# Performance work log

Hardware: AMD Instinct MI355X
Metric: run time of the kernel (lower is better)

Reference implementation:

```python
import jax, jax.numpy as jnp
import numpy as np

N = 8192
IN_F = 256
OUT_F = 256
ATTN_DIM = 2
NEG_INF = -1e18


def setup_inputs() -> dict:
    key = jax.random.key(0)
    k1, k2, k3, k4, k5 = jax.random.split(key, 5)
    node_feats = jax.random.normal(k1, (N, IN_F), dtype=jnp.float32)
    Ahat = (jax.random.uniform(k2, (N, N)) < 0.01).astype(jnp.float32)
    # ensure no isolated rows (self loops) so softmax rows are well-defined
    Ahat = Ahat.at[jnp.arange(N), jnp.arange(N)].set(1.0)
    bound_w = 1.0 / np.sqrt(IN_F)
    bound_wa = 1.0 / np.sqrt(OUT_F)
    bound_a = 1.0 / np.sqrt(2 * ATTN_DIM)
    w = jax.random.uniform(k3, (IN_F, OUT_F), minval=-bound_w, maxval=bound_w, dtype=jnp.float32)
    w_a = jax.random.uniform(k4, (OUT_F, ATTN_DIM), minval=-bound_wa, maxval=bound_wa, dtype=jnp.float32)
    a = jax.random.uniform(k5, (2 * ATTN_DIM, 1), minval=-bound_a, maxval=bound_a, dtype=jnp.float32)
    return {"node_feats": node_feats, "Ahat": Ahat, "w": w, "w_a": w_a, "a": a}


def reference(node_feats, Ahat, w, w_a, a):
    # h_prime: [N, out_features]
    h_prime = node_feats @ w
    # h_reduced: [N, attn_dim]
    h_reduced = h_prime @ w_a
    # e[i, j] = cat(h_red[i], h_red[j]) @ a  ==  h_red[i]@a[:d] + h_red[j]@a[d:]
    # (identical math to the repeat+cat+matmul in the original, without the
    #  O(N^2 * 2d) materialization)
    f_src = (h_reduced @ a[:ATTN_DIM]).squeeze(-1)  # [N]
    f_dst = (h_reduced @ a[ATTN_DIM:]).squeeze(-1)  # [N]
    e = f_src[:, None] + f_dst[None, :]             # [N, N]
    masked_e = jnp.where(Ahat > 0, e, NEG_INF)
    attn_scores = jax.nn.softmax(masked_e, axis=-1)  # [N, N]
    out = attn_scores @ h_prime                      # [N, out_features]
    return jax.nn.relu(out)
```

## Files before the change

### kernel.cpp

```cpp
#include <hip/hip_runtime.h>
#include <hip/hip_bf16.h>
#include <math.h>

#define NN 8192
#define IN_F 256
#define OUT_F 256

typedef _Float16 half4_t __attribute__((ext_vector_type(4)));
typedef float    f4_t    __attribute__((ext_vector_type(4)));

#define KC 32
#define LS 68

__global__ __launch_bounds__(256) void gemm_hprime(
    const float* __restrict__ X,
    const float* __restrict__ W,
    _Float16* __restrict__ H16)
{
    __shared__ float As[KC * LS];
    __shared__ float Bs[KC * LS];

    const int tid  = threadIdx.x;
    const int row0 = blockIdx.x * 64;
    const int col0 = blockIdx.y * 64;
    const int tx   = tid & 15;
    const int ty   = tid >> 4;

    float acc[4][4];
#pragma unroll
    for (int i = 0; i < 4; ++i)
#pragma unroll
        for (int j = 0; j < 4; ++j) acc[i][j] = 0.0f;

    for (int k0 = 0; k0 < IN_F; k0 += KC) {
        {
            const int k4 = tid & 7;
            const int r0 = tid >> 3;
#pragma unroll
            for (int rp = 0; rp < 2; ++rp) {
                const int r = r0 + rp * 32;
                const float4 v = *(const float4*)(X + (size_t)(row0 + r) * IN_F + k0 + k4 * 4);
                As[(k4 * 4 + 0) * LS + r] = v.x;
                As[(k4 * 4 + 1) * LS + r] = v.y;
                As[(k4 * 4 + 2) * LS + r] = v.z;
                As[(k4 * 4 + 3) * LS + r] = v.w;
            }
        }
        {
            const int c4 = tid & 15;
            const int kb = tid >> 4;
#pragma unroll
            for (int kp = 0; kp < 2; ++kp) {
                const int k = kb + kp * 16;
                *(float4*)(&Bs[k * LS + c4 * 4]) =
                    *(const float4*)(W + (size_t)(k0 + k) * OUT_F + col0 + c4 * 4);
            }
        }
        __syncthreads();

#pragma unroll
        for (int k = 0; k < KC; ++k) {
            const float4 av = *(const float4*)(&As[k * LS + ty * 4]);
            const float4 bv = *(const float4*)(&Bs[k * LS + tx * 4]);
            const float a_[4] = {av.x, av.y, av.z, av.w};
            const float b_[4] = {bv.x, bv.y, bv.z, bv.w};
#pragma unroll
            for (int i = 0; i < 4; ++i)
#pragma unroll
                for (int j = 0; j < 4; ++j)
                    acc[i][j] = fmaf(a_[i], b_[j], acc[i][j]);
        }
        __syncthreads();
    }

#pragma unroll
    for (int i = 0; i < 4; ++i) {
        half4_t o;
        o.x = (_Float16)acc[i][0];
        o.y = (_Float16)acc[i][1];
        o.z = (_Float16)acc[i][2];
        o.w = (_Float16)acc[i][3];
        *(half4_t*)(H16 + (size_t)(row0 + ty * 4 + i) * OUT_F + col0 + tx * 4) = o;
    }
}

__global__ __launch_bounds__(256) void fdst_exp(
    const _Float16* __restrict__ hp16,
    const float* __restrict__ w_a,
    const float* __restrict__ a,
    float* __restrict__ fexp)
{
    const int row  = blockIdx.x * 4 + (threadIdx.x >> 6);
    const int lane = threadIdx.x & 63;

    const float a2 = a[2];
    const float a3 = a[3];

    const half4_t h  = ((const half4_t*)hp16)[(size_t)row * 64 + lane];
    const float4 wa0 = *(const float4*)(w_a + lane * 8);
    const float4 wa1 = *(const float4*)(w_a + lane * 8 + 4);

    float s = (float)h.x * fmaf(wa0.x, a2, wa0.y * a3)
            + (float)h.y * fmaf(wa0.z, a2, wa0.w * a3)
            + (float)h.z * fmaf(wa1.x, a2, wa1.y * a3)
            + (float)h.w * fmaf(wa1.z, a2, wa1.w * a3);

#pragma unroll
    for (int off = 32; off > 0; off >>= 1) s += __shfl_xor(s, off, 64);

    if (lane == 0) fexp[row] = expf(s);
}

#define CAPW 192

__global__ __launch_bounds__(256) void attn_aggregate(
    const float* __restrict__ Ahat,
    const _Float16* __restrict__ hp16,
    const float* __restrict__ fexp,
    float* __restrict__ out)
{
    __shared__ int s_idx[4 * CAPW];

    const int wid  = threadIdx.x >> 6;
    const int lane = threadIdx.x & 63;
    const int row  = blockIdx.x * 4 + wid;
    int* const my_idx = s_idx + wid * CAPW;

    const f4_t* arow   = (const f4_t*)(Ahat + (size_t)row * NN);
    const half4_t* hp4 = (const half4_t*)hp16;

    int cnt = 0;
    f4_t v0 = __builtin_nontemporal_load(arow + lane);
    f4_t v1 = __builtin_nontemporal_load(arow + 64 + lane);

    for (int c = 0; c < 32; ++c) {
        const f4_t cur = v0;
        v0 = v1;
        if (c + 2 < 32) v1 = __builtin_nontemporal_load(arow + (c + 2) * 64 + lane);

        const int jbase = c * 256 + lane * 4;

#define COMPACT(pred, comp)                                                   \
        {                                                                     \
            const unsigned long long m = __ballot(pred);                      \
            const unsigned int lo = __builtin_amdgcn_mbcnt_lo((unsigned)m, 0);\
            const int pos = cnt + (int)__builtin_amdgcn_mbcnt_hi(             \
                                        (unsigned)(m >> 32), lo);             \
            if ((pred) && pos < CAPW) my_idx[pos] = jbase + (comp);           \
            cnt += __builtin_popcountll(m);                                   \
        }

        COMPACT(cur.x > 0.0f, 0)
        COMPACT(cur.y > 0.0f, 1)
        COMPACT(cur.z > 0.0f, 2)
        COMPACT(cur.w > 0.0f, 3)
#undef COMPACT
    }
    if (cnt > CAPW) cnt = CAPW;

    float4 acc = {0.0f, 0.0f, 0.0f, 0.0f};
    float den = 0.0f;

    int k = 0;
    for (; k + 8 <= cnt; k += 8) {
        const int4 ja = *(const int4*)(my_idx + k);
        const int4 jb = *(const int4*)(my_idx + k + 4);

        const float p0 = fexp[ja.x], p1 = fexp[ja.y], p2 = fexp[ja.z], p3 = fexp[ja.w];
        const float p4 = fexp[jb.x], p5 = fexp[jb.y], p6 = fexp[jb.z], p7 = fexp[jb.w];

        const half4_t h0 = hp4[((size_t)ja.x << 6) + lane];
        const half4_t h1 = hp4[((size_t)ja.y << 6) + lane];
        const half4_t h2 = hp4[((size_t)ja.z << 6) + lane];
        const half4_t h3 = hp4[((size_t)ja.w << 6) + lane];
        const half4_t h4 = hp4[((size_t)jb.x << 6) + lane];
        const half4_t h5 = hp4[((size_t)jb.y << 6) + lane];
        const half4_t h6 = hp4[((size_t)jb.z << 6) + lane];
        const half4_t h7 = hp4[((size_t)jb.w << 6) + lane];

        acc.x = fmaf(p0, (float)h0.x, acc.x); acc.y = fmaf(p0, (float)h0.y, acc.y);
        acc.z = fmaf(p0, (float)h0.z, acc.z); acc.w = fmaf(p0, (float)h0.w, acc.w);
        acc.x = fmaf(p1, (float)h1.x, acc.x); acc.y = fmaf(p1, (float)h1.y, acc.y);
        acc.z = fmaf(p1, (float)h1.z, acc.z); acc.w = fmaf(p1, (float)h1.w, acc.w);
        acc.x = fmaf(p2, (float)h2.x, acc.x); acc.y = fmaf(p2, (float)h2.y, acc.y);
        acc.z = fmaf(p2, (float)h2.z, acc.z); acc.w = fmaf(p2, (float)h2.w, acc.w);
        acc.x = fmaf(p3, (float)h3.x, acc.x); acc.y = fmaf(p3, (float)h3.y, acc.y);
        acc.z = fmaf(p3, (float)h3.z, acc.z); acc.w = fmaf(p3, (float)h3.w, acc.w);
        acc.x = fmaf(p4, (float)h4.x, acc.x); acc.y = fmaf(p4, (float)h4.y, acc.y);
        acc.z = fmaf(p4, (float)h4.z, acc.z); acc.w = fmaf(p4, (float)h4.w, acc.w);
        acc.x = fmaf(p5, (float)h5.x, acc.x); acc.y = fmaf(p5, (float)h5.y, acc.y);
        acc.z = fmaf(p5, (float)h5.z, acc.z); acc.w = fmaf(p5, (float)h5.w, acc.w);
        acc.x = fmaf(p6, (float)h6.x, acc.x); acc.y = fmaf(p6, (float)h6.y, acc.y);
        acc.z = fmaf(p6, (float)h6.z, acc.z); acc.w = fmaf(p6, (float)h6.w, acc.w);
        acc.x = fmaf(p7, (float)h7.x, acc.x); acc.y = fmaf(p7, (float)h7.y, acc.y);
        acc.z = fmaf(p7, (float)h7.z, acc.z); acc.w = fmaf(p7, (float)h7.w, acc.w);

        den += ((p0 + p1) + (p2 + p3)) + ((p4 + p5) + (p6 + p7));
    }
    for (; k < cnt; ++k) {
        const int j = my_idx[k];
        const float p = fexp[j];
        const half4_t h = hp4[((size_t)j << 6) + lane];
        acc.x = fmaf(p, (float)h.x, acc.x);
        acc.y = fmaf(p, (float)h.y, acc.y);
        acc.z = fmaf(p, (float)h.z, acc.z);
        acc.w = fmaf(p, (float)h.w, acc.w);
        den += p;
    }

    const float inv = 1.0f / den;
    float4 o;
    o.x = fmaxf(acc.x * inv, 0.0f);
    o.y = fmaxf(acc.y * inv, 0.0f);
    o.z = fmaxf(acc.z * inv, 0.0f);
    o.w = fmaxf(acc.w * inv, 0.0f);
    *(float4*)(out + (size_t)row * OUT_F + lane * 4) = o;
}

extern "C" void kernel_launch(void* const* d_in, const int* in_sizes, int n_in,
                              void* d_out, int out_size, void* d_ws, size_t ws_size,
                              hipStream_t stream) {
    const float* node_feats = (const float*)d_in[0];
    const float* Ahat       = (const float*)d_in[1];
    const float* w          = (const float*)d_in[2];
    const float* w_a        = (const float*)d_in[3];
    const float* a          = (const float*)d_in[4];
    float* out = (float*)d_out;

    _Float16* hp16 = (_Float16*)d_ws;
    float* fexp = (float*)(hp16 + (size_t)NN * OUT_F);

    gemm_hprime<<<dim3(NN / 64, OUT_F / 64), 256, 0, stream>>>(node_feats, w, hp16);
    fdst_exp<<<dim3(NN / 4), 256, 0, stream>>>(hp16, w_a, a, fexp);
    attn_aggregate<<<dim3(NN / 4), 256, 0, stream>>>(Ahat, hp16, fexp, out);
}
```

Baseline: 388.4 us.

## Run adjacency scan concurrently with the projection GEMM in one launch

The adjacency row scan and index compaction move out of the aggregation kernel into a combined launch. Its first 512 blocks compute the h_prime GEMM and the remaining blocks scan Ahat, writing compacted neighbour indices and counts to workspace. The scan also issues deeper prefetches, four float4 loads per lane ahead. The 256 MB Ahat read now overlaps the GEMM, and the gather kernel only reads small index lists. The cost is an extra global round-trip for the indices and a different block mix in the fused launch.

After: 397.6 us. +2.4%, slower.

```diff
diff --git a/kernel.cpp b/kernel.cpp
--- a/kernel.cpp
+++ b/kernel.cpp
@@ -11,77 +11,142 @@
 
 #define KC 32
 #define LS 68
-
-__global__ __launch_bounds__(256) void gemm_hprime(
+#define CAPW 192
+#define GEMM_BLOCKS 512
+#define SCAN_BLOCKS 2048
+
+__global__ __launch_bounds__(256) void scan_and_gemm(
+    const float* __restrict__ Ahat,
     const float* __restrict__ X,
     const float* __restrict__ W,
-    _Float16* __restrict__ H16)
+    _Float16* __restrict__ H16,
+    int* __restrict__ g_idx,
+    int* __restrict__ g_cnt)
 {
-    __shared__ float As[KC * LS];
-    __shared__ float Bs[KC * LS];
-
-    const int tid  = threadIdx.x;
-    const int row0 = blockIdx.x * 64;
-    const int col0 = blockIdx.y * 64;
-    const int tx   = tid & 15;
-    const int ty   = tid >> 4;
-
-    float acc[4][4];
-#pragma unroll
-    for (int i = 0; i < 4; ++i)
-#pragma unroll
-        for (int j = 0; j < 4; ++j) acc[i][j] = 0.0f;
-
-    for (int k0 = 0; k0 < IN_F; k0 += KC) {
-        {
-            const int k4 = tid & 7;
-            const int r0 = tid >> 3;
-#pragma unroll
-            for (int rp = 0; rp < 2; ++rp) {
-                const int r = r0 + rp * 32;
-                const float4 v = *(const float4*)(X + (size_t)(row0 + r) * IN_F + k0 + k4 * 4);
-                As[(k4 * 4 + 0) * LS + r] = v.x;
-                As[(k4 * 4 + 1) * LS + r] = v.y;
-                As[(k4 * 4 + 2) * LS + r] = v.z;
-                As[(k4 * 4 + 3) * LS + r] = v.w;
-            }
-        }
-        {
-            const int c4 = tid & 15;
-            const int kb = tid >> 4;
-#pragma unroll
-            for (int kp = 0; kp < 2; ++kp) {
-                const int k = kb + kp * 16;
-                *(float4*)(&Bs[k * LS + c4 * 4]) =
-                    *(const float4*)(W + (size_t)(k0 + k) * OUT_F + col0 + c4 * 4);
-            }
-        }
-        __syncthreads();
-
-#pragma unroll
-        for (int k = 0; k < KC; ++k) {
-            const float4 av = *(const float4*)(&As[k * LS + ty * 4]);
-            const float4 bv = *(const float4*)(&Bs[k * LS + tx * 4]);
-            const float a_[4] = {av.x, av.y, av.z, av.w};
-            const float b_[4] = {bv.x, bv.y, bv.z, bv.w};
-#pragma unroll
-            for (int i = 0; i < 4; ++i)
-#pragma unroll
-                for (int j = 0; j < 4; ++j)
-                    acc[i][j] = fmaf(a_[i], b_[j], acc[i][j]);
-        }
-        __syncthreads();
-    }
-
-#pragma unroll
-    for (int i = 0; i < 4; ++i) {
-        half4_t o;
-        o.x = (_Float16)acc[i][0];
-        o.y = (_Float16)acc[i][1];
-        o.z = (_Float16)acc[i][2];
-        o.w = (_Float16)acc[i][3];
-        *(half4_t*)(H16 + (size_t)(row0 + ty * 4 + i) * OUT_F + col0 + tx * 4) = o;
-    }
+    __shared__ float smem[2 * KC * LS];
+    const int bid = blockIdx.x;
+    const int tid = threadIdx.x;
+
+    if (bid < GEMM_BLOCKS) {
+        float* As = smem;
+        float* Bs = smem + KC * LS;
+        const int row0 = (bid & 127) * 64;
+        const int col0 = (bid >> 7) * 64;
+        const int tx = tid & 15;
+        const int ty = tid >> 4;
+
+        float acc[4][4];
+#pragma unroll
+        for (int i = 0; i < 4; ++i)
+#pragma unroll
+            for (int j = 0; j < 4; ++j) acc[i][j] = 0.0f;
+
+        for (int k0 = 0; k0 < IN_F; k0 += KC) {
+            {
+                const int k4 = tid & 7;
+                const int r0 = tid >> 3;
+#pragma unroll
+                for (int rp = 0; rp < 2; ++rp) {
+                    const int r = r0 + rp * 32;
+                    const float4 v = *(const float4*)(X + (size_t)(row0 + r) * IN_F + k0 + k4 * 4);
+                    As[(k4 * 4 + 0) * LS + r] = v.x;
+                    As[(k4 * 4 + 1) * LS + r] = v.y;
+                    As[(k4 * 4 + 2) * LS + r] = v.z;
+                    As[(k4 * 4 + 3) * LS + r] = v.w;
+                }
+            }
+            {
+                const int c4 = tid & 15;
+                const int kb = tid >> 4;
+#pragma unroll
+                for (int kp = 0; kp < 2; ++kp) {
+                    const int k = kb + kp * 16;
+                    *(float4*)(&Bs[k * LS + c4 * 4]) =
+                        *(const float4*)(W + (size_t)(k0 + k) * OUT_F + col0 + c4 * 4);
+                }
+            }
+            __syncthreads();
+
+#pragma unroll
+            for (int k = 0; k < KC; ++k) {
+                const float4 av = *(const float4*)(&As[k * LS + ty * 4]);
+                const float4 bv = *(const float4*)(&Bs[k * LS + tx * 4]);
+                const float a_[4] = {av.x, av.y, av.z, av.w};
+                const float b_[4] = {bv.x, bv.y, bv.z, bv.w};
+#pragma unroll
+                for (int i = 0; i < 4; ++i)
+#pragma unroll
+                    for (int j = 0; j < 4; ++j)
+                        acc[i][j] = fmaf(a_[i], b_[j], acc[i][j]);
+            }
+            __syncthreads();
+        }
+
+#pragma unroll
+        for (int i = 0; i < 4; ++i) {
+            half4_t o;
+            o.x = (_Float16)acc[i][0];
+            o.y = (_Float16)acc[i][1];
+            o.z = (_Float16)acc[i][2];
+            o.w = (_Float16)acc[i][3];
+            *(half4_t*)(H16 + (size_t)(row0 + ty * 4 + i) * OUT_F + col0 + tx * 4) = o;
+        }
+        return;
+    }
+
+    int* s_idx = (int*)smem;
+    const int wid  = tid >> 6;
+    const int lane = tid & 63;
+    const int row  = (bid - GEMM_BLOCKS) * 4 + wid;
+    int* const my_idx = s_idx + wid * CAPW;
+
+    const f4_t* arow = (const f4_t*)(Ahat + (size_t)row * NN);
+
+    int cnt = 0;
+    f4_t cur[4], nxt[4];
+#pragma unroll
+    for (int q = 0; q < 4; ++q)
+        cur[q] = __builtin_nontemporal_load(arow + q * 64 + lane);
+
+#pragma unroll
+    for (int g = 0; g < 8; ++g) {
+        if (g < 7) {
+#pragma unroll
+            for (int q = 0; q < 4; ++q)
+                nxt[q] = __builtin_nontemporal_load(arow + ((g + 1) * 4 + q) * 64 + lane);
+        }
+
+#pragma unroll
+        for (int q = 0; q < 4; ++q) {
+            const f4_t v = cur[q];
+            const int jbase = (g * 4 + q) * 256 + lane * 4;
+
+#define COMPACT(pred, comp)                                                   \
+            {                                                                 \
+                const unsigned long long m = __ballot(pred);                  \
+                const unsigned int lo =                                       \
+                    __builtin_amdgcn_mbcnt_lo((unsigned)m, 0);                \
+                const int pos = cnt + (int)__builtin_amdgcn_mbcnt_hi(         \
+                                            (unsigned)(m >> 32), lo);         \
+                if ((pred) && pos < CAPW) my_idx[pos] = jbase + (comp);       \
+                cnt += __builtin_popcountll(m);                               \
+            }
+
+            COMPACT(v.x > 0.0f, 0)
+            COMPACT(v.y > 0.0f, 1)
+            COMPACT(v.z > 0.0f, 2)
+            COMPACT(v.w > 0.0f, 3)
+#undef COMPACT
+        }
+
+#pragma unroll
+        for (int q = 0; q < 4; ++q) cur[q] = nxt[q];
+    }
+    if (cnt > CAPW) cnt = CAPW;
+
+    for (int k = lane; k < cnt; k += 64)
+        g_idx[(size_t)row * CAPW + k] = my_idx[k];
+    if (lane == 0) g_cnt[row] = cnt;
 }
 
 __global__ __launch_bounds__(256) void fdst_exp(
@@ -111,60 +176,28 @@
     if (lane == 0) fexp[row] = expf(s);
 }
 
-#define CAPW 192
-
-__global__ __launch_bounds__(256) void attn_aggregate(
-    const float* __restrict__ Ahat,
+__global__ __launch_bounds__(256) void gather_aggregate(
     const _Float16* __restrict__ hp16,
     const float* __restrict__ fexp,
+    const int* __restrict__ g_idx,
+    const int* __restrict__ g_cnt,
     float* __restrict__ out)
 {
-    __shared__ int s_idx[4 * CAPW];
-
     const int wid  = threadIdx.x >> 6;
     const int lane = threadIdx.x & 63;
     const int row  = blockIdx.x * 4 + wid;
-    int* const my_idx = s_idx + wid * CAPW;
-
-    const f4_t* arow   = (const f4_t*)(Ahat + (size_t)row * NN);
+
+    const int cnt = g_cnt[row];
+    const int* idx = g_idx + (size_t)row * CAPW;
     const half4_t* hp4 = (const half4_t*)hp16;
-
-    int cnt = 0;
-    f4_t v0 = __builtin_nontemporal_load(arow + lane);
-    f4_t v1 = __builtin_nontemporal_load(arow + 64 + lane);
-
-    for (int c = 0; c < 32; ++c) {
-        const f4_t cur = v0;
-        v0 = v1;
-        if (c + 2 < 32) v1 = __builtin_nontemporal_load(arow + (c + 2) * 64 + lane);
-
-        const int jbase = c * 256 + lane * 4;
-
-#define COMPACT(pred, comp)                                                   \
-        {                                                                     \
-            const unsigned long long m = __ballot(pred);                      \
-            const unsigned int lo = __builtin_amdgcn_mbcnt_lo((unsigned)m, 0);\
-            const int pos = cnt + (int)__builtin_amdgcn_mbcnt_hi(             \
-                                        (unsigned)(m >> 32), lo);             \
-            if ((pred) && pos < CAPW) my_idx[pos] = jbase + (comp);           \
-            cnt += __builtin_popcountll(m);                                   \
-        }
-
-        COMPACT(cur.x > 0.0f, 0)
-        COMPACT(cur.y > 0.0f, 1)
-        COMPACT(cur.z > 0.0f, 2)
-        COMPACT(cur.w > 0.0f, 3)
-#undef COMPACT
-    }
-    if (cnt > CAPW) cnt = CAPW;
 
     float4 acc = {0.0f, 0.0f, 0.0f, 0.0f};
     float den = 0.0f;
 
     int k = 0;
     for (; k + 8 <= cnt; k += 8) {
-        const int4 ja = *(const int4*)(my_idx + k);
-        const int4 jb = *(const int4*)(my_idx + k + 4);
+        const int4 ja = *(const int4*)(idx + k);
+        const int4 jb = *(const int4*)(idx + k + 4);
 
         const float p0 = fexp[ja.x], p1 = fexp[ja.y], p2 = fexp[ja.z], p3 = fexp[ja.w];
         const float p4 = fexp[jb.x], p5 = fexp[jb.y], p6 = fexp[jb.z], p7 = fexp[jb.w];
@@ -198,7 +231,7 @@
         den += ((p0 + p1) + (p2 + p3)) + ((p4 + p5) + (p6 + p7));
     }
     for (; k < cnt; ++k) {
-        const int j = my_idx[k];
+        const int j = idx[k];
         const float p = fexp[j];
         const half4_t h = hp4[((size_t)j << 6) + lane];
         acc.x = fmaf(p, (float)h.x, acc.x);
@@ -227,10 +260,16 @@
     const float* a          = (const float*)d_in[4];
     float* out = (float*)d_out;
 
-    _Float16* hp16 = (_Float16*)d_ws;
-    float* fexp = (float*)(hp16 + (size_t)NN * OUT_F);
-
-    gemm_hprime<<<dim3(NN / 64, OUT_F / 64), 256, 0, stream>>>(node_feats, w, hp16);
+    char* ws = (char*)d_ws;
+    _Float16* hp16 = (_Float16*)ws;
+    float* fexp    = (float*)(ws + 4194304);
+    int* g_cnt     = (int*)(ws + 4194304 + 32768);
+    int* g_idx     = (int*)(ws + 4194304 + 65536);
+
+    scan_and_gemm<<<dim3(GEMM_BLOCKS + SCAN_BLOCKS), 256, 0, stream>>>(
+        Ahat, node_feats, w, hp16, g_idx, g_cnt);
+
     fdst_exp<<<dim3(NN / 4), 256, 0, stream>>>(hp16, w_a, a, fexp);
-    attn_aggregate<<<dim3(NN / 4), 256, 0, stream>>>(Ahat, hp16, fexp, out);
-}
+
+    gather_aggregate<<<dim3(NN / 4), 256, 0, stream>>>(hp16, fexp, g_idx, g_cnt, out);
+}
```
